# Optimization experiments

Hardware: AMD Instinct MI355X
Metric: run time of the kernel (lower is better)

## Reference

```python
import jax, jax.numpy as jnp
import numpy as np
import math

HIDDEN = 128; NHEADS = 4; N_COE = 50; N_SCALES = 4; THRE = 5.0; S = 4096; B = 1


def setup_inputs():
    key = jax.random.key(0)
    ks = jax.random.split(key, 12)
    w = lambda k, shape: jax.random.normal(k, shape, jnp.float32) * 0.05
    return {
        "eigenvalue": jax.random.uniform(ks[0], (B, S), jnp.float32) * 2.0,  # graph Laplacian eigvals in [0,2)
        "length": jnp.full((B,), S, dtype=jnp.int32),
        "sele_num": jnp.full((B,), S, dtype=jnp.int32),
        "eig_w_W": w(ks[1], (HIDDEN + 1, HIDDEN)), "eig_w_b": jnp.zeros((HIDDEN,), jnp.float32),
        "mha_ln_g": jnp.ones((HIDDEN,), jnp.float32), "mha_ln_b": jnp.zeros((HIDDEN,), jnp.float32),
        "in_W": w(ks[2], (HIDDEN, 3 * HIDDEN)), "in_b": jnp.zeros((3 * HIDDEN,), jnp.float32),
        "out_W": w(ks[3], (HIDDEN, HIDDEN)), "out_b": jnp.zeros((HIDDEN,), jnp.float32),
        "ffn_ln_g": jnp.ones((HIDDEN,), jnp.float32), "ffn_ln_b": jnp.zeros((HIDDEN,), jnp.float32),
        "ffn1_W": w(ks[4], (HIDDEN, HIDDEN)), "ffn1_b": jnp.zeros((HIDDEN,), jnp.float32),
        "ffn2_W": w(ks[5], (HIDDEN, HIDDEN)), "ffn2_b": jnp.zeros((HIDDEN,), jnp.float32),
        "dsc_W": w(ks[6], (HIDDEN, N_COE)), "dsc_b": jnp.zeros((N_COE,), jnp.float32),
        "dwv_W": w(ks[7], (HIDDEN, N_COE)), "dwv_b": jnp.zeros((N_COE,), jnp.float32),
        "dss_W": w(ks[8], (HIDDEN, N_SCALES)), "dss_b": jnp.zeros((N_SCALES,), jnp.float32),
    }


def layer_norm(x, g, b, eps=1e-5):
    m = x.mean(-1, keepdims=True)
    v = ((x - m) ** 2).mean(-1, keepdims=True)
    return (x - m) / jnp.sqrt(v + eps) * g + b


def sine_encoding(e, W, b):
    # e: [B, S] -> [B, S, HIDDEN]
    div = jnp.exp(jnp.arange(0, HIDDEN, 2, dtype=e.dtype) * (-math.log(10000.0) / HIDDEN))
    pe = (e * 100.0)[..., None] * div  # [B, S, HIDDEN/2]
    eeig = jnp.concatenate([e[..., None], jnp.sin(pe), jnp.cos(pe)], axis=-1)  # [B, S, HIDDEN+1]
    return eeig @ W + b


def mha(x, pad_mask, in_W, in_b, out_W, out_b):
    # x: [B, S, D]; pad_mask: [B, S] True = masked key
    Bb, Ss, D = x.shape
    hd = D // NHEADS
    qkv = x @ in_W + in_b
    q, k, v = jnp.split(qkv, 3, axis=-1)
    hsplit = lambda t: t.reshape(Bb, Ss, NHEADS, hd).transpose(0, 2, 1, 3)  # [B, H, S, hd]
    q, k, v = hsplit(q), hsplit(k), hsplit(v)
    scores = jnp.einsum('bhqd,bhkd->bhqk', q, k) / math.sqrt(hd)
    scores = jnp.where(pad_mask[:, None, None, :], -jnp.inf, scores)
    attn = jax.nn.softmax(scores, axis=-1)
    o = jnp.einsum('bhqk,bhkd->bhqd', attn, v).transpose(0, 2, 1, 3).reshape(Bb, Ss, D)
    return o @ out_W + out_b


def cheb_base(y, n_coe, flag):
    # Chebyshev recurrence: wavelet = [T_0, T_2, ...], scaling = [T_1, T_3, ...]
    te0 = jnp.ones_like(y)
    to0 = y
    def step(carry, _):
        te, to = carry
        te = 2.0 * y * to - te
        to = 2.0 * y * te - to
        return (te, to), (te, to)
    _, (evens, odds) = jax.lax.scan(step, (te0, to0), None, length=n_coe - 1)
    if flag == 'scaling':
        base = jnp.concatenate([to0[None], odds], axis=0)   # [n_coe, B, S, d]
    else:
        base = jnp.concatenate([te0[None], evens], axis=0)
    return jnp.moveaxis(base, 0, 1)  # [B, n_coe, S, d]


def _forward(eigenvalue, eig_w_W, eig_w_b, mha_ln_g, mha_ln_b, in_W, in_b, out_W, out_b,
             ffn_ln_g, ffn_ln_b, ffn1_W, ffn1_b, ffn2_W, ffn2_b,
             dsc_W, dsc_b, dwv_W, dwv_b, dss_W, dss_b, length, sele_num):
    Bb, Ss = eigenvalue.shape
    eve = eigenvalue
    eig_mask = jnp.arange(Ss)[None, :] >= sele_num[:, None]  # [B, S] True = pad
    # --- EigenEncoding (dropout in eval mode = identity) ---
    eig = sine_encoding(eve, eig_w_W, eig_w_b)
    eig = eig + mha(layer_norm(eig, mha_ln_g, mha_ln_b), eig_mask, in_W, in_b, out_W, out_b)
    f = layer_norm(eig, ffn_ln_g, ffn_ln_b)
    f = jax.nn.gelu(f @ ffn1_W + ffn1_b, approximate=False) @ ffn2_W + ffn2_b
    eig_filter = eig + f  # [B, S, HIDDEN]
    lenf = length.astype(eve.dtype)[:, None]
    def pooled(W, b):
        c = eig_filter @ W + b
        c = jnp.where(eig_mask[..., None], 0.0, c)
        return c.sum(axis=1) / (lenf + 1e-8)
    coe_scaling = jax.nn.sigmoid(pooled(dsc_W, dsc_b))
    coe_scaling = coe_scaling / (coe_scaling.sum(-1, keepdims=True) + 1e-8)  # [B, n_coe]
    coe_wavelet = jax.nn.sigmoid(pooled(dwv_W, dwv_b))
    coe_wavelet = coe_wavelet / (coe_wavelet.sum(-1, keepdims=True) + 1e-8)
    coe_scales = jax.nn.sigmoid(pooled(dss_W, dss_b)) * THRE  # [B, n_scales]
    # --- Chebyshev bases ---
    base_scaling = cheb_base(eve[..., None] - 1.0, N_COE, 'scaling')  # [B, n_coe, S, 1]
    fsw = eve[..., None] * coe_scales[:, None, :]                      # [B, S, n_scales]
    fsw = jnp.where(fsw > 2.0, 0.0, fsw)
    base_wavelet = cheb_base(fsw - 1.0, N_COE, 'wavelet')             # [B, n_coe, S, n_scales]
    base_scaling = 0.5 * (1.0 - base_scaling)
    base_wavelet = 0.5 * (1.0 - base_wavelet)
    curr_scaling = jnp.einsum('bc,bcsd->bsd', coe_scaling, base_scaling)
    curr_wavelet = jnp.einsum('bc,bcsd->bsd', coe_wavelet, base_wavelet)
    out = jnp.concatenate([curr_scaling, curr_wavelet], axis=-1)       # [B, S, 1+n_scales]
    out = out / (jnp.linalg.norm(out, axis=-1, keepdims=True) + 1e-8)  # cfg.lam.tight_use = True
    return out


def reference(eigenvalue, length, sele_num, eig_w_W, eig_w_b, mha_ln_g, mha_ln_b, in_W, in_b,
              out_W, out_b, ffn_ln_g, ffn_ln_b, ffn1_W, ffn1_b, ffn2_W, ffn2_b,
              dsc_W, dsc_b, dwv_W, dwv_b, dss_W, dss_b):
    return _forward(eigenvalue, eig_w_W, eig_w_b, mha_ln_g, mha_ln_b, in_W, in_b, out_W, out_b,
                    ffn_ln_g, ffn_ln_b, ffn1_W, ffn1_b, ffn2_W, ffn2_b,
                    dsc_W, dsc_b, dwv_W, dwv_b, dss_W, dss_b, length, sele_num)
```

## Files before the change

### kernel.cpp

```cpp
#include <hip/hip_runtime.h>
#include <math.h>


#define SLOTS 8

typedef __attribute__((ext_vector_type(8))) short short8;
typedef __attribute__((ext_vector_type(4))) short short4v;
typedef __attribute__((ext_vector_type(4))) float f32x4;

__device__ inline unsigned short f2bf(float x) {
    unsigned u = __float_as_uint(x);
    return (unsigned short)((u + 0x7FFFu + ((u >> 16) & 1u)) >> 16);
}
__device__ inline float bf2f(unsigned short h) { return __uint_as_float(((unsigned)h) << 16); }

__global__ __launch_bounds__(256) void k_embed(const float* __restrict__ eve,
    const float* __restrict__ eigW, const float* __restrict__ ebias,
    const float* __restrict__ g, const float* __restrict__ b,
    const float* __restrict__ inW, const float* __restrict__ inb,
    float* __restrict__ eig, float* __restrict__ qkv, unsigned short* __restrict__ Khi_g,
    unsigned short* __restrict__ Klo_g, unsigned short* __restrict__ Vt_g)
{
    __shared__ __align__(16) float wsh[129 * 128];
    __shared__ __align__(16) float se[16][132];
    __shared__ __align__(16) float xn[16][132];
    __shared__ __align__(16) unsigned short vsh[128][16];
    const int t = threadIdx.x;
    const int r0 = blockIdx.x * 16;
    {
        const int r = t >> 4, l4 = t & 15;
        const float e = eve[r0 + r];
        if (l4 == 0) se[r][128] = e;
        #pragma unroll
        for (int jj = 0; jj < 4; ++jj) {
            const int j = l4 * 4 + jj;
            const float div = __expf(-0.07195578415606394f * (float)(2 * j));
            const float pe = e * 100.0f * div;
            se[r][j]      = __sinf(pe);
            se[r][64 + j] = __cosf(pe);
        }
    }
    {
        const float4* __restrict__ src = (const float4*)eigW;
        float4* dst = (float4*)wsh;
        #pragma unroll
        for (int i = 0; i < 17; ++i) {
            const int f = t + i * 256;
            if (f < 4128) dst[f] = src[f];
        }
    }
    __syncthreads();
    const int lane = t & 63;
    const int w = t >> 6;
    const int rp = w * 2 + (lane >> 5);
    const int c0 = (lane & 31) * 4;
    const int ra = rp * 2, rb = ra + 1;
    float xa[4], xb[4];
    {
        const float4 w0 = *(const float4*)&wsh[c0];
        const float ea = se[ra][128], eb = se[rb][128];
        float a0 = ea * w0.x, a1 = ea * w0.y, a2 = ea * w0.z, a3 = ea * w0.w;
        float b0 = eb * w0.x, b1 = eb * w0.y, b2 = eb * w0.z, b3 = eb * w0.w;
        #pragma unroll 8
        for (int k = 0; k < 128; ++k) {
            const float xva = se[ra][k];
            const float xvb = se[rb][k];
            const float4 wk = *(const float4*)&wsh[(k + 1) * 128 + c0];
            a0 = fmaf(xva, wk.x, a0); a1 = fmaf(xva, wk.y, a1);
            a2 = fmaf(xva, wk.z, a2); a3 = fmaf(xva, wk.w, a3);
            b0 = fmaf(xvb, wk.x, b0); b1 = fmaf(xvb, wk.y, b1);
            b2 = fmaf(xvb, wk.z, b2); b3 = fmaf(xvb, wk.w, b3);
        }
        const float4 bb = *(const float4*)&ebias[c0];
        xa[0] = a0 + bb.x; xa[1] = a1 + bb.y; xa[2] = a2 + bb.z; xa[3] = a3 + bb.w;
        xb[0] = b0 + bb.x; xb[1] = b1 + bb.y; xb[2] = b2 + bb.z; xb[3] = b3 + bb.w;
        *(float4*)&eig[(size_t)(r0 + ra) * 128 + c0] = make_float4(xa[0], xa[1], xa[2], xa[3]);
        *(float4*)&eig[(size_t)(r0 + rb) * 128 + c0] = make_float4(xb[0], xb[1], xb[2], xb[3]);
    }
    {
        float sa = (xa[0] + xa[1]) + (xa[2] + xa[3]);
        float qa = (xa[0] * xa[0] + xa[1] * xa[1]) + (xa[2] * xa[2] + xa[3] * xa[3]);
        float sb = (xb[0] + xb[1]) + (xb[2] + xb[3]);
        float qb = (xb[0] * xb[0] + xb[1] * xb[1]) + (xb[2] * xb[2] + xb[3] * xb[3]);
        #pragma unroll
        for (int m = 1; m < 32; m <<= 1) {
            sa += __shfl_xor(sa, m, 32); qa += __shfl_xor(qa, m, 32);
            sb += __shfl_xor(sb, m, 32); qb += __shfl_xor(qb, m, 32);
        }
        const float ma = sa * (1.f / 128.f), mb = sb * (1.f / 128.f);
        const float ia = 1.f / sqrtf(qa * (1.f / 128.f) - ma * ma + 1e-5f);
        const float ib = 1.f / sqrtf(qb * (1.f / 128.f) - mb * mb + 1e-5f);
        const float4 gg = *(const float4*)&g[c0];
        const float4 bb = *(const float4*)&b[c0];
        *(float4*)&xn[ra][c0] = make_float4((xa[0] - ma) * ia * gg.x + bb.x,
                                            (xa[1] - ma) * ia * gg.y + bb.y,
                                            (xa[2] - ma) * ia * gg.z + bb.z,
                                            (xa[3] - ma) * ia * gg.w + bb.w);
        *(float4*)&xn[rb][c0] = make_float4((xb[0] - mb) * ib * gg.x + bb.x,
                                            (xb[1] - mb) * ib * gg.y + bb.y,
                                            (xb[2] - mb) * ib * gg.z + bb.z,
                                            (xb[3] - mb) * ib * gg.w + bb.w);
    }
    const int rowa = r0 + ra, rowb = r0 + rb;
    for (int p = 0; p < 3; ++p) {
        __syncthreads();
        {
            const float4* __restrict__ src = (const float4*)inW;
            float4* dst = (float4*)wsh;
            #pragma unroll
            for (int i = 0; i < 16; ++i) {
                const int f = t + i * 256;
                const int k = f >> 5, c4 = f & 31;
                dst[f] = src[k * 96 + p * 32 + c4];
            }
        }
        __syncthreads();
        float A[4], B[4];
        {
            const float4 bb = *(const float4*)&inb[p * 128 + c0];
            A[0] = bb.x; A[1] = bb.y; A[2] = bb.z; A[3] = bb.w;
            B[0] = bb.x; B[1] = bb.y; B[2] = bb.z; B[3] = bb.w;
        }
        #pragma unroll 8
        for (int k = 0; k < 128; ++k) {
            const float xva = xn[ra][k];
            const float xvb = xn[rb][k];
            const float4 wk = *(const float4*)&wsh[k * 128 + c0];
            A[0] = fmaf(xva, wk.x, A[0]); A[1] = fmaf(xva, wk.y, A[1]);
            A[2] = fmaf(xva, wk.z, A[2]); A[3] = fmaf(xva, wk.w, A[3]);
            B[0] = fmaf(xvb, wk.x, B[0]); B[1] = fmaf(xvb, wk.y, B[1]);
            B[2] = fmaf(xvb, wk.z, B[2]); B[3] = fmaf(xvb, wk.w, B[3]);
        }
        if (p == 0) {
            *(float4*)&qkv[(size_t)rowa * 384 + c0] = make_float4(A[0], A[1], A[2], A[3]);
            *(float4*)&qkv[(size_t)rowb * 384 + c0] = make_float4(B[0], B[1], B[2], B[3]);
        } else if (p == 1) {
            const int h = c0 >> 5, d = c0 & 31;
            unsigned short h4[4], l4v[4];
            #pragma unroll
            for (int i = 0; i < 4; ++i) { h4[i] = f2bf(A[i]); l4v[i] = f2bf(A[i] - bf2f(h4[i])); }
            *(uint2*)&Khi_g[((size_t)h * 4096 + rowa) * 32 + d] = *(uint2*)h4;
            *(uint2*)&Klo_g[((size_t)h * 4096 + rowa) * 32 + d] = *(uint2*)l4v;
            #pragma unroll
            for (int i = 0; i < 4; ++i) { h4[i] = f2bf(B[i]); l4v[i] = f2bf(B[i] - bf2f(h4[i])); }
            *(uint2*)&Khi_g[((size_t)h * 4096 + rowb) * 32 + d] = *(uint2*)h4;
            *(uint2*)&Klo_g[((size_t)h * 4096 + rowb) * 32 + d] = *(uint2*)l4v;
        } else {
            #pragma unroll
            for (int i = 0; i < 4; ++i) {
                vsh[c0 + i][ra] = f2bf(A[i]);
                vsh[c0 + i][rb] = f2bf(B[i]);
            }
        }
    }
    __syncthreads();
    if (t < 128) {
        const uint4 v0 = *(const uint4*)&vsh[t][0];
        const uint4 v1 = *(const uint4*)&vsh[t][8];
        *(uint4*)&Vt_g[(size_t)t * 4096 + r0]     = v0;
        *(uint4*)&Vt_g[(size_t)t * 4096 + r0 + 8] = v1;
    }
}

#define PSTR 72

__global__ __launch_bounds__(256) void k_attn(const float* __restrict__ qkv,
    const unsigned short* __restrict__ Khi_g, const unsigned short* __restrict__ Klo_g,
    const unsigned short* __restrict__ Vt_g,
    const int* __restrict__ sele, float* __restrict__ Oe, float* __restrict__ E)
{
    __shared__ __align__(16) unsigned short Pb[4][64 * PSTR];

    const int t = threadIdx.x;
    const int lane = t & 63;
    const int l = lane & 15;
    const int quad = lane >> 4;
    const int wv = __builtin_amdgcn_readfirstlane(t >> 6);
    const int qb = blockIdx.x;
    const int h  = blockIdx.y;
    const int slot = blockIdx.z * 4 + wv;
    const int nk = sele[0];
    unsigned short* __restrict__ Pw = Pb[wv];

    short8 qhi[4], qlo[4];
    #pragma unroll
    for (int qf = 0; qf < 4; ++qf) {
        const float* __restrict__ qr =
            qkv + (size_t)(qb * 64 + qf * 16 + l) * 384 + h * 32 + quad * 8;
        const float4 a = *(const float4*)qr;
        const float4 b = *(const float4*)(qr + 4);
        const float sc = 0.17677669529663687f;
        float v[8] = {a.x * sc, a.y * sc, a.z * sc, a.w * sc, b.x * sc, b.y * sc, b.z * sc, b.w * sc};
        #pragma unroll
        for (int j = 0; j < 8; ++j) {
            const unsigned short hb = f2bf(v[j]);
            qhi[qf][j] = (short)hb;
            qlo[qf][j] = (short)f2bf(v[j] - bf2f(hb));
        }
    }
    f32x4 accO[4][2];
    #pragma unroll
    for (int qf = 0; qf < 4; ++qf) {
        accO[qf][0] = (f32x4){0.f, 0.f, 0.f, 0.f};
        accO[qf][1] = (f32x4){0.f, 0.f, 0.f, 0.f};
    }
    float elane[4] = {0.f, 0.f, 0.f, 0.f};

    for (int ch = 0; ch < 8; ++ch) {
        const int keybase = slot * 512 + ch * 64;
        #pragma unroll
        for (int tile = 0; tile < 4; ++tile) {
            const size_t krow = (size_t)h * 4096 + keybase + tile * 16 + l;
            const short8 kh = *(const short8*)&Khi_g[krow * 32 + quad * 8];
            const short8 kw = *(const short8*)&Klo_g[krow * 32 + quad * 8];
            const int kg0 = keybase + tile * 16 + quad * 4;
            #pragma unroll
            for (int qf = 0; qf < 4; ++qf) {
                f32x4 S = {0.f, 0.f, 0.f, 0.f};
                S = __builtin_amdgcn_mfma_f32_16x16x32_bf16(kh, qhi[qf], S, 0, 0, 0);
                S = __builtin_amdgcn_mfma_f32_16x16x32_bf16(kw, qhi[qf], S, 0, 0, 0);
                S = __builtin_amdgcn_mfma_f32_16x16x32_bf16(kh, qlo[qf], S, 0, 0, 0);
                short4v pw;
                #pragma unroll
                for (int r = 0; r < 4; ++r) {
                    const float p = (kg0 + r < nk) ? __expf(S[r]) : 0.f;
                    elane[qf] += p;
                    pw[r] = (short)f2bf(p);
                }
                *(short4v*)&Pw[(qf * 16 + l) * PSTR + tile * 16 + quad * 4] = pw;
            }
        }
        #pragma unroll
        for (int pair = 0; pair < 2; ++pair) {
            short8 pa[4];
            #pragma unroll
            for (int qf = 0; qf < 4; ++qf)
                pa[qf] = *(const short8*)&Pw[(qf * 16 + l) * PSTR + pair * 32 + quad * 8];
            #pragma unroll
            for (int dt = 0; dt < 2; ++dt) {
                const short8 vb = *(const short8*)
                    &Vt_g[((size_t)h * 32 + dt * 16 + l) * 4096 + keybase + pair * 32 + quad * 8];
                #pragma unroll
                for (int qf = 0; qf < 4; ++qf)
                    accO[qf][dt] = __builtin_amdgcn_mfma_f32_16x16x32_bf16(pa[qf], vb, accO[qf][dt], 0, 0, 0);
            }
        }
    }
    #pragma unroll
    for (int qf = 0; qf < 4; ++qf) {
        float e = elane[qf];
        e += __shfl_xor(e, 16, 64);
        e += __shfl_xor(e, 32, 64);
        if (lane < 16)
            E[((size_t)slot * 4 + h) * 4096 + qb * 64 + qf * 16 + l] = e;
        #pragma unroll
        for (int r = 0; r < 4; ++r) {
            const size_t row = qb * 64 + qf * 16 + quad * 4 + r;
            Oe[((size_t)slot * 4096 + row) * 128 + h * 32 + l]      = accO[qf][0][r];
            Oe[((size_t)slot * 4096 + row) * 128 + h * 32 + 16 + l] = accO[qf][1][r];
        }
    }
}

__global__ __launch_bounds__(256) void k_ffn(const float* __restrict__ eig,
    const float* __restrict__ Oe, const float* __restrict__ E,
    const float* __restrict__ outW, const float* __restrict__ outb,
    const float* __restrict__ lg, const float* __restrict__ lb,
    const float* __restrict__ W1, const float* __restrict__ b1,
    const float* __restrict__ W2, const float* __restrict__ b2,
    const int* __restrict__ sele, float* __restrict__ xsum)
{
    __shared__ __align__(16) float wsh[128 * 128];
    __shared__ __align__(16) float sA[16][132];
    __shared__ __align__(16) float xn[16][132];
    __shared__ __align__(16) float cs[16][132];
    const int t = threadIdx.x;
    const int r0 = blockIdx.x * 16;
    {
        const int r = t >> 4, c8 = (t & 15) * 8;
        const int h = c8 >> 5;
        float es = 0.f;
        float v[8] = {0.f, 0.f, 0.f, 0.f, 0.f, 0.f, 0.f, 0.f};
        #pragma unroll
        for (int ks = 0; ks < SLOTS; ++ks) {
            es += E[((size_t)ks * 4 + h) * 4096 + r0 + r];
            const float4 o1 = *(const float4*)&Oe[((size_t)ks * 4096 + r0 + r) * 128 + c8];
            const float4 o2 = *(const float4*)&Oe[((size_t)ks * 4096 + r0 + r) * 128 + c8 + 4];
            v[0] += o1.x; v[1] += o1.y; v[2] += o1.z; v[3] += o1.w;
            v[4] += o2.x; v[5] += o2.y; v[6] += o2.z; v[7] += o2.w;
        }
        const float rcp = 1.f / es;
        *(float4*)&sA[r][c8]     = make_float4(v[0] * rcp, v[1] * rcp, v[2] * rcp, v[3] * rcp);
        *(float4*)&sA[r][c8 + 4] = make_float4(v[4] * rcp, v[5] * rcp, v[6] * rcp, v[7] * rcp);
    }
    {
        const float4* __restrict__ src = (const float4*)outW;
        float4* dst = (float4*)wsh;
        #pragma unroll
        for (int i = 0; i < 16; ++i) dst[t + i * 256] = src[t + i * 256];
    }
    __syncthreads();
    const int lane = t & 63;
    const int w = t >> 6;
    const int rp = w * 2 + (lane >> 5);
    const int c0 = (lane & 31) * 4;
    const int ra = rp * 2, rb = ra + 1;
    float x2a[4], x2b[4];
    {
        const float4 bb = *(const float4*)&outb[c0];
        float a0 = bb.x, a1 = bb.y, a2 = bb.z, a3 = bb.w;
        float b0 = bb.x, b1 = bb.y, b2 = bb.z, b3 = bb.w;
        #pragma unroll 8
        for (int k = 0; k < 128; ++k) {
            const float xva = sA[ra][k];
            const float xvb = sA[rb][k];
            const float4 wk = *(const float4*)&wsh[k * 128 + c0];
            a0 = fmaf(xva, wk.x, a0); a1 = fmaf(xva, wk.y, a1);
            a2 = fmaf(xva, wk.z, a2); a3 = fmaf(xva, wk.w, a3);
            b0 = fmaf(xvb, wk.x, b0); b1 = fmaf(xvb, wk.y, b1);
            b2 = fmaf(xvb, wk.z, b2); b3 = fmaf(xvb, wk.w, b3);
        }
        const float4 ea = *(const float4*)&eig[(size_t)(r0 + ra) * 128 + c0];
        const float4 eb = *(const float4*)&eig[(size_t)(r0 + rb) * 128 + c0];
        x2a[0] = ea.x + a0; x2a[1] = ea.y + a1; x2a[2] = ea.z + a2; x2a[3] = ea.w + a3;
        x2b[0] = eb.x + b0; x2b[1] = eb.y + b1; x2b[2] = eb.z + b2; x2b[3] = eb.w + b3;
    }
    {
        float sa = (x2a[0] + x2a[1]) + (x2a[2] + x2a[3]);
        float qa = (x2a[0] * x2a[0] + x2a[1] * x2a[1]) + (x2a[2] * x2a[2] + x2a[3] * x2a[3]);
        float sb = (x2b[0] + x2b[1]) + (x2b[2] + x2b[3]);
        float qb = (x2b[0] * x2b[0] + x2b[1] * x2b[1]) + (x2b[2] * x2b[2] + x2b[3] * x2b[3]);
        #pragma unroll
        for (int m = 1; m < 32; m <<= 1) {
            sa += __shfl_xor(sa, m, 32); qa += __shfl_xor(qa, m, 32);
            sb += __shfl_xor(sb, m, 32); qb += __shfl_xor(qb, m, 32);
        }
        const float ma = sa * (1.f / 128.f), mb = sb * (1.f / 128.f);
        const float ia = 1.f / sqrtf(qa * (1.f / 128.f) - ma * ma + 1e-5f);
        const float ib = 1.f / sqrtf(qb * (1.f / 128.f) - mb * mb + 1e-5f);
        const float4 gg = *(const float4*)&lg[c0];
        const float4 bb = *(const float4*)&lb[c0];
        *(float4*)&xn[ra][c0] = make_float4((x2a[0] - ma) * ia * gg.x + bb.x,
                                            (x2a[1] - ma) * ia * gg.y + bb.y,
                                            (x2a[2] - ma) * ia * gg.z + bb.z,
                                            (x2a[3] - ma) * ia * gg.w + bb.w);
        *(float4*)&xn[rb][c0] = make_float4((x2b[0] - mb) * ib * gg.x + bb.x,
                                            (x2b[1] - mb) * ib * gg.y + bb.y,
                                            (x2b[2] - mb) * ib * gg.z + bb.z,
                                            (x2b[3] - mb) * ib * gg.w + bb.w);
    }
    __syncthreads();
    {
        const float4* __restrict__ src = (const float4*)W1;
        float4* dst = (float4*)wsh;
        #pragma unroll
        for (int i = 0; i < 16; ++i) dst[t + i * 256] = src[t + i * 256];
    }
    __syncthreads();
    {
        const float4 bb = *(const float4*)&b1[c0];
        float a0 = bb.x, a1 = bb.y, a2 = bb.z, a3 = bb.w;
        float b0 = bb.x, b1v = bb.y, b2v = bb.z, b3 = bb.w;
        #pragma unroll 8
        for (int k = 0; k < 128; ++k) {
            const float xva = xn[ra][k];
            const float xvb = xn[rb][k];
            const float4 wk = *(const float4*)&wsh[k * 128 + c0];
            a0 = fmaf(xva, wk.x, a0); a1 = fmaf(xva, wk.y, a1);
            a2 = fmaf(xva, wk.z, a2); a3 = fmaf(xva, wk.w, a3);
            b0 = fmaf(xvb, wk.x, b0); b1v = fmaf(xvb, wk.y, b1v);
            b2v = fmaf(xvb, wk.z, b2v); b3 = fmaf(xvb, wk.w, b3);
        }
        *(float4*)&sA[ra][c0] = make_float4(
            0.5f * a0 * (1.f + erff(a0 * 0.70710678118654752f)),
            0.5f * a1 * (1.f + erff(a1 * 0.70710678118654752f)),
            0.5f * a2 * (1.f + erff(a2 * 0.70710678118654752f)),
            0.5f * a3 * (1.f + erff(a3 * 0.70710678118654752f)));
        *(float4*)&sA[rb][c0] = make_float4(
            0.5f * b0 * (1.f + erff(b0 * 0.70710678118654752f)),
            0.5f * b1v * (1.f + erff(b1v * 0.70710678118654752f)),
            0.5f * b2v * (1.f + erff(b2v * 0.70710678118654752f)),
            0.5f * b3 * (1.f + erff(b3 * 0.70710678118654752f)));
    }
    __syncthreads();
    {
        const float4* __restrict__ src = (const float4*)W2;
        float4* dst = (float4*)wsh;
        #pragma unroll
        for (int i = 0; i < 16; ++i) dst[t + i * 256] = src[t + i * 256];
    }
    __syncthreads();
    {
        const float4 bb = *(const float4*)&b2[c0];
        float a0 = bb.x, a1 = bb.y, a2 = bb.z, a3 = bb.w;
        float b0 = bb.x, b1v = bb.y, b2v = bb.z, b3 = bb.w;
        #pragma unroll 8
        for (int k = 0; k < 128; ++k) {
            const float xva = sA[ra][k];
            const float xvb = sA[rb][k];
            const float4 wk = *(const float4*)&wsh[k * 128 + c0];
            a0 = fmaf(xva, wk.x, a0); a1 = fmaf(xva, wk.y, a1);
            a2 = fmaf(xva, wk.z, a2); a3 = fmaf(xva, wk.w, a3);
            b0 = fmaf(xvb, wk.x, b0); b1v = fmaf(xvb, wk.y, b1v);
            b2v = fmaf(xvb, wk.z, b2v); b3 = fmaf(xvb, wk.w, b3);
        }
        const int nsel = sele[0];
        const bool ina = (r0 + ra) < nsel, inb2 = (r0 + rb) < nsel;
        *(float4*)&cs[ra][c0] = ina ? make_float4(x2a[0] + a0, x2a[1] + a1, x2a[2] + a2, x2a[3] + a3)
                                    : make_float4(0.f, 0.f, 0.f, 0.f);
        *(float4*)&cs[rb][c0] = inb2 ? make_float4(x2b[0] + b0, x2b[1] + b1v, x2b[2] + b2v, x2b[3] + b3)
                                     : make_float4(0.f, 0.f, 0.f, 0.f);
    }
    __syncthreads();
    if (t < 128) {
        float s = 0.f;
        #pragma unroll
        for (int rr = 0; rr < 16; ++rr) s += cs[rr][t];
        atomicAdd(&xsum[t], s);
    }
}

__global__ __launch_bounds__(512) void k_coef(const float* __restrict__ xsum,
    const float* __restrict__ dscW, const float* __restrict__ dscb,
    const float* __restrict__ dwvW, const float* __restrict__ dwvb,
    const float* __restrict__ dssW, const float* __restrict__ dssb,
    const int* __restrict__ len, const int* __restrict__ sele,
    float* __restrict__ coef)
{
    __shared__ float xs[128];
    __shared__ float part[104][4];
    __shared__ float val[104];
    __shared__ float s2[2];
    const int t = threadIdx.x;
    if (t < 128) xs[t] = xsum[t];
    __syncthreads();
    const float invl = 1.f / ((float)len[0] + 1e-8f);
    const float ns = (float)sele[0];
    const int o = t >> 2, lk = t & 3;
    if (o < 104) {
        const float* Wp; int stride, col;
        if (o < 50)       { Wp = dscW; stride = 50; col = o; }
        else if (o < 100) { Wp = dwvW; stride = 50; col = o - 50; }
        else              { Wp = dssW; stride = 4;  col = o - 100; }
        float a = 0.f;
        #pragma unroll
        for (int kk = 0; kk < 32; ++kk) {
            const int k = lk * 32 + kk;
            a = fmaf(xs[k], Wp[k * stride + col], a);
        }
        part[o][lk] = a;
    }
    __syncthreads();
    if (t < 104) {
        const float bias = (t < 50) ? dscb[t] : ((t < 100) ? dwvb[t - 50] : dssb[t - 100]);
        float a = ((part[t][0] + part[t][1]) + (part[t][2] + part[t][3]) + ns * bias) * invl;
        val[t] = 1.f / (1.f + __expf(-a));
    }
    __syncthreads();
    if (t == 0) { float s = 0.f; for (int i = 0; i < 50; ++i) s += val[i]; s2[0] = s; }
    if (t == 1) { float s = 0.f; for (int i = 0; i < 50; ++i) s += val[50 + i]; s2[1] = s; }
    __syncthreads();
    if (t < 50) {
        coef[t]      = val[t] / (s2[0] + 1e-8f);
        coef[50 + t] = val[50 + t] / (s2[1] + 1e-8f);
    } else if (t >= 100 && t < 104) {
        coef[t] = val[t] * 5.0f;
    }
}

__global__ __launch_bounds__(128) void k_out(const float* __restrict__ eve,
    const float* __restrict__ coef, float* __restrict__ out)
{
    __shared__ float csc[50], cwv[50], cssh[4];
    const int t = threadIdx.x;
    if (t < 50) csc[t] = coef[t];
    else if (t < 100) cwv[t - 50] = coef[t];
    else if (t < 104) cssh[t - 100] = coef[t];
    __syncthreads();
    const int s = blockIdx.x * 128 + t;
    const float e = eve[s];
    float vals[5];
    {
        const float y = e - 1.f;
        float te = 1.f, to = y;
        float a = csc[0] * (0.5f * (1.f - to));
        const float y2 = 2.f * y;
        for (int i = 1; i < 50; ++i) {
            te = fmaf(y2, to, -te);
            to = fmaf(y2, te, -to);
            a = fmaf(csc[i], 0.5f * (1.f - to), a);
        }
        vals[0] = a;
    }
    #pragma unroll
    for (int j = 0; j < 4; ++j) {
        float f = e * cssh[j];
        if (f > 2.f) f = 0.f;
        const float y = f - 1.f;
        float te = 1.f, to = y;
        float a = cwv[0] * (0.5f * (1.f - te));
        const float y2 = 2.f * y;
        for (int i = 1; i < 50; ++i) {
            te = fmaf(y2, to, -te);
            to = fmaf(y2, te, -to);
            a = fmaf(cwv[i], 0.5f * (1.f - te), a);
        }
        vals[1 + j] = a;
    }
    float n2 = 0.f;
    #pragma unroll
    for (int k = 0; k < 5; ++k) n2 += vals[k] * vals[k];
    const float invn = 1.f / (sqrtf(n2) + 1e-8f);
    #pragma unroll
    for (int k = 0; k < 5; ++k) out[s * 5 + k] = vals[k] * invn;
}

extern "C" void kernel_launch(void* const* d_in, const int* in_sizes, int n_in,
                              void* d_out, int out_size, void* d_ws, size_t ws_size,
                              hipStream_t stream) {
    const float* eve  = (const float*)d_in[0];
    const int*   len  = (const int*)d_in[1];
    const int*   sele = (const int*)d_in[2];
    const float* eigW = (const float*)d_in[3];
    const float* eigB = (const float*)d_in[4];
    const float* mlg  = (const float*)d_in[5];
    const float* mlb  = (const float*)d_in[6];
    const float* inW  = (const float*)d_in[7];
    const float* inb  = (const float*)d_in[8];
    const float* outW = (const float*)d_in[9];
    const float* outb = (const float*)d_in[10];
    const float* flg  = (const float*)d_in[11];
    const float* flb  = (const float*)d_in[12];
    const float* W1   = (const float*)d_in[13];
    const float* b1   = (const float*)d_in[14];
    const float* W2   = (const float*)d_in[15];
    const float* b2   = (const float*)d_in[16];
    const float* dscW = (const float*)d_in[17];
    const float* dscb = (const float*)d_in[18];
    const float* dwvW = (const float*)d_in[19];
    const float* dwvb = (const float*)d_in[20];
    const float* dssW = (const float*)d_in[21];
    const float* dssb = (const float*)d_in[22];

    float* ws   = (float*)d_ws;
    float* eig  = ws;
    float* qkv  = ws + 524288;
    float* Oe   = ws + 2097152;
    float* E    = ws + 6291456;
    float* xsum = ws + 6422528;
    float* coef = ws + 6422656;
    unsigned short* Khi_g = (unsigned short*)(ws + 6422784);
    unsigned short* Klo_g = (unsigned short*)(ws + 6684928);
    unsigned short* Vt_g  = (unsigned short*)(ws + 6947072);
    float* out  = (float*)d_out;

    hipMemsetAsync(xsum, 0, 128 * sizeof(float), stream);
    k_embed<<<256, 256, 0, stream>>>(eve, eigW, eigB, mlg, mlb, inW, inb,
                                     eig, qkv, Khi_g, Klo_g, Vt_g);
    k_attn <<<dim3(64, 4, 2), 256, 0, stream>>>(qkv, Khi_g, Klo_g, Vt_g, sele, Oe, E);
    k_ffn  <<<256, 256, 0, stream>>>(eig, Oe, E, outW, outb, flg, flb, W1, b1, W2, b2, sele, xsum);
    k_coef <<<1, 512, 0, stream>>>(xsum, dscW, dscb, dwvW, dwvb, dssW, dssb, len, sele, coef);
    k_out  <<<32, 128, 0, stream>>>(eve, coef, out);
}
```

Baseline: 190.5 us.

## Halve rows per block in embed/FFN and double attention key split

Embed and FFN kernels now handle 8 rows per block with one row per thread group, so each launch has twice as many blocks (512). Attention splits the keys into 16 slots of 256 instead of 8 of 512, with grid z doubled, and the workspace layout is grown to hold the larger partial-output buffer. The goal is more blocks to fill the GPU's compute units. The cost is that each block reloads the weight matrices for half as many rows, and FFN must read and sum twice as many partial attention outputs.

```diff
diff --git a/kernel.cpp b/kernel.cpp
--- a/kernel.cpp
+++ b/kernel.cpp
@@ -2,7 +2,7 @@
 #include <math.h>
 
 
-#define SLOTS 8
+#define SLOTS 16
 
 typedef __attribute__((ext_vector_type(8))) short short8;
 typedef __attribute__((ext_vector_type(4))) short short4v;
@@ -22,18 +22,20 @@
     unsigned short* __restrict__ Klo_g, unsigned short* __restrict__ Vt_g)
 {
     __shared__ __align__(16) float wsh[129 * 128];
-    __shared__ __align__(16) float se[16][132];
-    __shared__ __align__(16) float xn[16][132];
-    __shared__ __align__(16) unsigned short vsh[128][16];
+    __shared__ __align__(16) float se[8][132];
+    __shared__ __align__(16) float xn[8][132];
+    __shared__ __align__(16) unsigned short vsh[128][8];
     const int t = threadIdx.x;
-    const int r0 = blockIdx.x * 16;
-    {
-        const int r = t >> 4, l4 = t & 15;
+    const int r0 = blockIdx.x * 8;
+    const int r = t >> 5;
+    const int l = t & 31;
+    const int c0 = l * 4;
+    {
         const float e = eve[r0 + r];
-        if (l4 == 0) se[r][128] = e;
-        #pragma unroll
-        for (int jj = 0; jj < 4; ++jj) {
-            const int j = l4 * 4 + jj;
+        if (l == 0) se[r][128] = e;
+        #pragma unroll
+        for (int jj = 0; jj < 2; ++jj) {
+            const int j = l * 2 + jj;
             const float div = __expf(-0.07195578415606394f * (float)(2 * j));
             const float pe = e * 100.0f * div;
             se[r][j]      = __sinf(pe);
@@ -50,58 +52,37 @@
         }
     }
     __syncthreads();
-    const int lane = t & 63;
-    const int w = t >> 6;
-    const int rp = w * 2 + (lane >> 5);
-    const int c0 = (lane & 31) * 4;
-    const int ra = rp * 2, rb = ra + 1;
-    float xa[4], xb[4];
+    float xa[4];
     {
         const float4 w0 = *(const float4*)&wsh[c0];
-        const float ea = se[ra][128], eb = se[rb][128];
-        float a0 = ea * w0.x, a1 = ea * w0.y, a2 = ea * w0.z, a3 = ea * w0.w;
-        float b0 = eb * w0.x, b1 = eb * w0.y, b2 = eb * w0.z, b3 = eb * w0.w;
+        const float e = se[r][128];
+        float a0 = e * w0.x, a1 = e * w0.y, a2 = e * w0.z, a3 = e * w0.w;
         #pragma unroll 8
         for (int k = 0; k < 128; ++k) {
-            const float xva = se[ra][k];
-            const float xvb = se[rb][k];
+            const float xv = se[r][k];
             const float4 wk = *(const float4*)&wsh[(k + 1) * 128 + c0];
-            a0 = fmaf(xva, wk.x, a0); a1 = fmaf(xva, wk.y, a1);
-            a2 = fmaf(xva, wk.z, a2); a3 = fmaf(xva, wk.w, a3);
-            b0 = fmaf(xvb, wk.x, b0); b1 = fmaf(xvb, wk.y, b1);
-            b2 = fmaf(xvb, wk.z, b2); b3 = fmaf(xvb, wk.w, b3);
+            a0 = fmaf(xv, wk.x, a0); a1 = fmaf(xv, wk.y, a1);
+            a2 = fmaf(xv, wk.z, a2); a3 = fmaf(xv, wk.w, a3);
         }
         const float4 bb = *(const float4*)&ebias[c0];
         xa[0] = a0 + bb.x; xa[1] = a1 + bb.y; xa[2] = a2 + bb.z; xa[3] = a3 + bb.w;
-        xb[0] = b0 + bb.x; xb[1] = b1 + bb.y; xb[2] = b2 + bb.z; xb[3] = b3 + bb.w;
-        *(float4*)&eig[(size_t)(r0 + ra) * 128 + c0] = make_float4(xa[0], xa[1], xa[2], xa[3]);
-        *(float4*)&eig[(size_t)(r0 + rb) * 128 + c0] = make_float4(xb[0], xb[1], xb[2], xb[3]);
-    }
-    {
-        float sa = (xa[0] + xa[1]) + (xa[2] + xa[3]);
-        float qa = (xa[0] * xa[0] + xa[1] * xa[1]) + (xa[2] * xa[2] + xa[3] * xa[3]);
-        float sb = (xb[0] + xb[1]) + (xb[2] + xb[3]);
-        float qb = (xb[0] * xb[0] + xb[1] * xb[1]) + (xb[2] * xb[2] + xb[3] * xb[3]);
-        #pragma unroll
-        for (int m = 1; m < 32; m <<= 1) {
-            sa += __shfl_xor(sa, m, 32); qa += __shfl_xor(qa, m, 32);
-            sb += __shfl_xor(sb, m, 32); qb += __shfl_xor(qb, m, 32);
-        }
-        const float ma = sa * (1.f / 128.f), mb = sb * (1.f / 128.f);
-        const float ia = 1.f / sqrtf(qa * (1.f / 128.f) - ma * ma + 1e-5f);
-        const float ib = 1.f / sqrtf(qb * (1.f / 128.f) - mb * mb + 1e-5f);
+        *(float4*)&eig[(size_t)(r0 + r) * 128 + c0] = make_float4(xa[0], xa[1], xa[2], xa[3]);
+    }
+    {
+        float s = (xa[0] + xa[1]) + (xa[2] + xa[3]);
+        float q = (xa[0] * xa[0] + xa[1] * xa[1]) + (xa[2] * xa[2] + xa[3] * xa[3]);
+        #pragma unroll
+        for (int m = 1; m < 32; m <<= 1) { s += __shfl_xor(s, m, 32); q += __shfl_xor(q, m, 32); }
+        const float mean = s * (1.f / 128.f);
+        const float inv  = 1.f / sqrtf(q * (1.f / 128.f) - mean * mean + 1e-5f);
         const float4 gg = *(const float4*)&g[c0];
         const float4 bb = *(const float4*)&b[c0];
-        *(float4*)&xn[ra][c0] = make_float4((xa[0] - ma) * ia * gg.x + bb.x,
-                                            (xa[1] - ma) * ia * gg.y + bb.y,
-                                            (xa[2] - ma) * ia * gg.z + bb.z,
-                                            (xa[3] - ma) * ia * gg.w + bb.w);
-        *(float4*)&xn[rb][c0] = make_float4((xb[0] - mb) * ib * gg.x + bb.x,
-                                            (xb[1] - mb) * ib * gg.y + bb.y,
-                                            (xb[2] - mb) * ib * gg.z + bb.z,
-                                            (xb[3] - mb) * ib * gg.w + bb.w);
-    }
-    const int rowa = r0 + ra, rowb = r0 + rb;
+        *(float4*)&xn[r][c0] = make_float4((xa[0] - mean) * inv * gg.x + bb.x,
+                                           (xa[1] - mean) * inv * gg.y + bb.y,
+                                           (xa[2] - mean) * inv * gg.z + bb.z,
+                                           (xa[3] - mean) * inv * gg.w + bb.w);
+    }
+    const int row = r0 + r;
     for (int p = 0; p < 3; ++p) {
         __syncthreads();
         {
@@ -115,50 +96,37 @@
             }
         }
         __syncthreads();
-        float A[4], B[4];
+        float A[4];
         {
             const float4 bb = *(const float4*)&inb[p * 128 + c0];
             A[0] = bb.x; A[1] = bb.y; A[2] = bb.z; A[3] = bb.w;
-            B[0] = bb.x; B[1] = bb.y; B[2] = bb.z; B[3] = bb.w;
         }
         #pragma unroll 8
         for (int k = 0; k < 128; ++k) {
-            const float xva = xn[ra][k];
-            const float xvb = xn[rb][k];
+            const float xv = xn[r][k];
             const float4 wk = *(const float4*)&wsh[k * 128 + c0];
-            A[0] = fmaf(xva, wk.x, A[0]); A[1] = fmaf(xva, wk.y, A[1]);
-            A[2] = fmaf(xva, wk.z, A[2]); A[3] = fmaf(xva, wk.w, A[3]);
-            B[0] = fmaf(xvb, wk.x, B[0]); B[1] = fmaf(xvb, wk.y, B[1]);
-            B[2] = fmaf(xvb, wk.z, B[2]); B[3] = fmaf(xvb, wk.w, B[3]);
+            A[0] = fmaf(xv, wk.x, A[0]); A[1] = fmaf(xv, wk.y, A[1]);
+            A[2] = fmaf(xv, wk.z, A[2]); A[3] = fmaf(xv, wk.w, A[3]);
         }
         if (p == 0) {
-            *(float4*)&qkv[(size_t)rowa * 384 + c0] = make_float4(A[0], A[1], A[2], A[3]);
-            *(float4*)&qkv[(size_t)rowb * 384 + c0] = make_float4(B[0], B[1], B[2], B[3]);
+            *(float4*)&qkv[(size_t)row * 384 + c0] = make_float4(A[0], A[1], A[2], A[3]);
         } else if (p == 1) {
             const int h = c0 >> 5, d = c0 & 31;
             unsigned short h4[4], l4v[4];
             #pragma unroll
             for (int i = 0; i < 4; ++i) { h4[i] = f2bf(A[i]); l4v[i] = f2bf(A[i] - bf2f(h4[i])); }
-            *(uint2*)&Khi_g[((size_t)h * 4096 + rowa) * 32 + d] = *(uint2*)h4;
-            *(uint2*)&Klo_g[((size_t)h * 4096 + rowa) * 32 + d] = *(uint2*)l4v;
-            #pragma unroll
-            for (int i = 0; i < 4; ++i) { h4[i] = f2bf(B[i]); l4v[i] = f2bf(B[i] - bf2f(h4[i])); }
-            *(uint2*)&Khi_g[((size_t)h * 4096 + rowb) * 32 + d] = *(uint2*)h4;
-            *(uint2*)&Klo_g[((size_t)h * 4096 + rowb) * 32 + d] = *(uint2*)l4v;
+            *(uint2*)&Khi_g[((size_t)h * 4096 + row) * 32 + d] = *(uint2*)h4;
+            *(uint2*)&Klo_g[((size_t)h * 4096 + row) * 32 + d] = *(uint2*)l4v;
         } else {
             #pragma unroll
-            for (int i = 0; i < 4; ++i) {
-                vsh[c0 + i][ra] = f2bf(A[i]);
-                vsh[c0 + i][rb] = f2bf(B[i]);
-            }
+            for (int i = 0; i < 4; ++i)
+                vsh[c0 + i][r] = f2bf(A[i]);
         }
     }
     __syncthreads();
     if (t < 128) {
         const uint4 v0 = *(const uint4*)&vsh[t][0];
-        const uint4 v1 = *(const uint4*)&vsh[t][8];
-        *(uint4*)&Vt_g[(size_t)t * 4096 + r0]     = v0;
-        *(uint4*)&Vt_g[(size_t)t * 4096 + r0 + 8] = v1;
+        *(uint4*)&Vt_g[(size_t)t * 4096 + r0] = v0;
     }
 }
 
@@ -206,8 +174,8 @@
     }
     float elane[4] = {0.f, 0.f, 0.f, 0.f};
 
-    for (int ch = 0; ch < 8; ++ch) {
-        const int keybase = slot * 512 + ch * 64;
+    for (int ch = 0; ch < 4; ++ch) {
+        const int keybase = slot * 256 + ch * 64;
         #pragma unroll
         for (int tile = 0; tile < 4; ++tile) {
             const size_t krow = (size_t)h * 4096 + keybase + tile * 16 + l;
@@ -271,27 +239,26 @@
     const int* __restrict__ sele, float* __restrict__ xsum)
 {
     __shared__ __align__(16) float wsh[128 * 128];
-    __shared__ __align__(16) float sA[16][132];
-    __shared__ __align__(16) float xn[16][132];
-    __shared__ __align__(16) float cs[16][132];
+    __shared__ __align__(16) float sA[8][132];
+    __shared__ __align__(16) float xn[8][132];
+    __shared__ __align__(16) float cs[8][132];
     const int t = threadIdx.x;
-    const int r0 = blockIdx.x * 16;
-    {
-        const int r = t >> 4, c8 = (t & 15) * 8;
-        const int h = c8 >> 5;
+    const int r0 = blockIdx.x * 8;
+    const int r = t >> 5;
+    const int c0 = (t & 31) * 4;
+    const int row = r0 + r;
+    {
+        const int h = c0 >> 5;
         float es = 0.f;
-        float v[8] = {0.f, 0.f, 0.f, 0.f, 0.f, 0.f, 0.f, 0.f};
+        float v[4] = {0.f, 0.f, 0.f, 0.f};
         #pragma unroll
         for (int ks = 0; ks < SLOTS; ++ks) {
-            es += E[((size_t)ks * 4 + h) * 4096 + r0 + r];
-            const float4 o1 = *(const float4*)&Oe[((size_t)ks * 4096 + r0 + r) * 128 + c8];
-            const float4 o2 = *(const float4*)&Oe[((size_t)ks * 4096 + r0 + r) * 128 + c8 + 4];
+            es += E[((size_t)ks * 4 + h) * 4096 + row];
+            const float4 o1 = *(const float4*)&Oe[((size_t)ks * 4096 + row) * 128 + c0];
             v[0] += o1.x; v[1] += o1.y; v[2] += o1.z; v[3] += o1.w;
-            v[4] += o2.x; v[5] += o2.y; v[6] += o2.z; v[7] += o2.w;
         }
         const float rcp = 1.f / es;
-        *(float4*)&sA[r][c8]     = make_float4(v[0] * rcp, v[1] * rcp, v[2] * rcp, v[3] * rcp);
-        *(float4*)&sA[r][c8 + 4] = make_float4(v[4] * rcp, v[5] * rcp, v[6] * rcp, v[7] * rcp);
+        *(float4*)&sA[r][c0] = make_float4(v[0] * rcp, v[1] * rcp, v[2] * rcp, v[3] * rcp);
     }
     {
         const float4* __restrict__ src = (const float4*)outW;
@@ -300,54 +267,33 @@
         for (int i = 0; i < 16; ++i) dst[t + i * 256] = src[t + i * 256];
     }
     __syncthreads();
-    const int lane = t & 63;
-    const int w = t >> 6;
-    const int rp = w * 2 + (lane >> 5);
-    const int c0 = (lane & 31) * 4;
-    const int ra = rp * 2, rb = ra + 1;
-    float x2a[4], x2b[4];
+    float x2[4];
     {
         const float4 bb = *(const float4*)&outb[c0];
         float a0 = bb.x, a1 = bb.y, a2 = bb.z, a3 = bb.w;
-        float b0 = bb.x, b1 = bb.y, b2 = bb.z, b3 = bb.w;
         #pragma unroll 8
         for (int k = 0; k < 128; ++k) {
-            const float xva = sA[ra][k];
-            const float xvb = sA[rb][k];
+            const float xv = sA[r][k];
             const float4 wk = *(const float4*)&wsh[k * 128 + c0];
-            a0 = fmaf(xva, wk.x, a0); a1 = fmaf(xva, wk.y, a1);
-            a2 = fmaf(xva, wk.z, a2); a3 = fmaf(xva, wk.w, a3);
-            b0 = fmaf(xvb, wk.x, b0); b1 = fmaf(xvb, wk.y, b1);
-            b2 = fmaf(xvb, wk.z, b2); b3 = fmaf(xvb, wk.w, b3);
-        }
-        const float4 ea = *(const float4*)&eig[(size_t)(r0 + ra) * 128 + c0];
-        const float4 eb = *(const float4*)&eig[(size_t)(r0 + rb) * 128 + c0];
-        x2a[0] = ea.x + a0; x2a[1] = ea.y + a1; x2a[2] = ea.z + a2; x2a[3] = ea.w + a3;
-        x2b[0] = eb.x + b0; x2b[1] = eb.y + b1; x2b[2] = eb.z + b2; x2b[3] = eb.w + b3;
-    }
-    {
-        float sa = (x2a[0] + x2a[1]) + (x2a[2] + x2a[3]);
-        float qa = (x2a[0] * x2a[0] + x2a[1] * x2a[1]) + (x2a[2] * x2a[2] + x2a[3] * x2a[3]);
-        float sb = (x2b[0] + x2b[1]) + (x2b[2] + x2b[3]);
-        float qb = (x2b[0] * x2b[0] + x2b[1] * x2b[1]) + (x2b[2] * x2b[2] + x2b[3] * x2b[3]);
-        #pragma unroll
-        for (int m = 1; m < 32; m <<= 1) {
-            sa += __shfl_xor(sa, m, 32); qa += __shfl_xor(qa, m, 32);
-            sb += __shfl_xor(sb, m, 32); qb += __shfl_xor(qb, m, 32);
-        }
-        const float ma = sa * (1.f / 128.f), mb = sb * (1.f / 128.f);
-        const float ia = 1.f / sqrtf(qa * (1.f / 128.f) - ma * ma + 1e-5f);
-        const float ib = 1.f / sqrtf(qb * (1.f / 128.f) - mb * mb + 1e-5f);
+            a0 = fmaf(xv, wk.x, a0); a1 = fmaf(xv, wk.y, a1);
+            a2 = fmaf(xv, wk.z, a2); a3 = fmaf(xv, wk.w, a3);
+        }
+        const float4 ea = *(const float4*)&eig[(size_t)row * 128 + c0];
+        x2[0] = ea.x + a0; x2[1] = ea.y + a1; x2[2] = ea.z + a2; x2[3] = ea.w + a3;
+    }
+    {
+        float s = (x2[0] + x2[1]) + (x2[2] + x2[3]);
+        float q = (x2[0] * x2[0] + x2[1] * x2[1]) + (x2[2] * x2[2] + x2[3] * x2[3]);
+        #pragma unroll
+        for (int m = 1; m < 32; m <<= 1) { s += __shfl_xor(s, m, 32); q += __shfl_xor(q, m, 32); }
+        const float mean = s * (1.f / 128.f);
+        const float inv  = 1.f / sqrtf(q * (1.f / 128.f) - mean * mean + 1e-5f);
         const float4 gg = *(const float4*)&lg[c0];
         const float4 bb = *(const float4*)&lb[c0];
-        *(float4*)&xn[ra][c0] = make_float4((x2a[0] - ma) * ia * gg.x + bb.x,
-                                            (x2a[1] - ma) * ia * gg.y + bb.y,
-                                            (x2a[2] - ma) * ia * gg.z + bb.z,
-                                            (x2a[3] - ma) * ia * gg.w + bb.w);
-        *(float4*)&xn[rb][c0] = make_float4((x2b[0] - mb) * ib * gg.x + bb.x,
-                                            (x2b[1] - mb) * ib * gg.y + bb.y,
-                                            (x2b[2] - mb) * ib * gg.z + bb.z,
-                                            (x2b[3] - mb) * ib * gg.w + bb.w);
+        *(float4*)&xn[r][c0] = make_float4((x2[0] - mean) * inv * gg.x + bb.x,
+                                           (x2[1] - mean) * inv * gg.y + bb.y,
+                                           (x2[2] - mean) * inv * gg.z + bb.z,
+                                           (x2[3] - mean) * inv * gg.w + bb.w);
     }
     __syncthreads();
     {
@@ -360,27 +306,18 @@
     {
         const float4 bb = *(const float4*)&b1[c0];
         float a0 = bb.x, a1 = bb.y, a2 = bb.z, a3 = bb.w;
-        float b0 = bb.x, b1v = bb.y, b2v = bb.z, b3 = bb.w;
         #pragma unroll 8
         for (int k = 0; k < 128; ++k) {
-            const float xva = xn[ra][k];
-            const float xvb = xn[rb][k];
+            const float xv = xn[r][k];
             const float4 wk = *(const float4*)&wsh[k * 128 + c0];
-            a0 = fmaf(xva, wk.x, a0); a1 = fmaf(xva, wk.y, a1);
-            a2 = fmaf(xva, wk.z, a2); a3 = fmaf(xva, wk.w, a3);
-            b0 = fmaf(xvb, wk.x, b0); b1v = fmaf(xvb, wk.y, b1v);
-            b2v = fmaf(xvb, wk.z, b2v); b3 = fmaf(xvb, wk.w, b3);
-        }
-        *(float4*)&sA[ra][c0] = make_float4(
+            a0 = fmaf(xv, wk.x, a0); a1 = fmaf(xv, wk.y, a1);
+            a2 = fmaf(xv, wk.z, a2); a3 = fmaf(xv, wk.w, a3);
+        }
+        *(float4*)&sA[r][c0] = make_float4(
             0.5f * a0 * (1.f + erff(a0 * 0.70710678118654752f)),
             0.5f * a1 * (1.f + erff(a1 * 0.70710678118654752f)),
             0.5f * a2 * (1.f + erff(a2 * 0.70710678118654752f)),
             0.5f * a3 * (1.f + erff(a3 * 0.70710678118654752f)));
-        *(float4*)&sA[rb][c0] = make_float4(
-            0.5f * b0 * (1.f + erff(b0 * 0.70710678118654752f)),
-            0.5f * b1v * (1.f + erff(b1v * 0.70710678118654752f)),
-            0.5f * b2v * (1.f + erff(b2v * 0.70710678118654752f)),
-            0.5f * b3 * (1.f + erff(b3 * 0.70710678118654752f)));
     }
     __syncthreads();
     {
@@ -393,29 +330,22 @@
     {
         const float4 bb = *(const float4*)&b2[c0];
         float a0 = bb.x, a1 = bb.y, a2 = bb.z, a3 = bb.w;
-        float b0 = bb.x, b1v = bb.y, b2v = bb.z, b3 = bb.w;
         #pragma unroll 8
         for (int k = 0; k < 128; ++k) {
-            const float xva = sA[ra][k];
-            const float xvb = sA[rb][k];
+            const float xv = sA[r][k];
             const float4 wk = *(const float4*)&wsh[k * 128 + c0];
-            a0 = fmaf(xva, wk.x, a0); a1 = fmaf(xva, wk.y, a1);
-            a2 = fmaf(xva, wk.z, a2); a3 = fmaf(xva, wk.w, a3);
-            b0 = fmaf(xvb, wk.x, b0); b1v = fmaf(xvb, wk.y, b1v);
-            b2v = fmaf(xvb, wk.z, b2v); b3 = fmaf(xvb, wk.w, b3);
-        }
-        const int nsel = sele[0];
-        const bool ina = (r0 + ra) < nsel, inb2 = (r0 + rb) < nsel;
-        *(float4*)&cs[ra][c0] = ina ? make_float4(x2a[0] + a0, x2a[1] + a1, x2a[2] + a2, x2a[3] + a3)
-                                    : make_float4(0.f, 0.f, 0.f, 0.f);
-        *(float4*)&cs[rb][c0] = inb2 ? make_float4(x2b[0] + b0, x2b[1] + b1v, x2b[2] + b2v, x2b[3] + b3)
-                                     : make_float4(0.f, 0.f, 0.f, 0.f);
+            a0 = fmaf(xv, wk.x, a0); a1 = fmaf(xv, wk.y, a1);
+            a2 = fmaf(xv, wk.z, a2); a3 = fmaf(xv, wk.w, a3);
+        }
+        const bool in = row < sele[0];
+        *(float4*)&cs[r][c0] = in ? make_float4(x2[0] + a0, x2[1] + a1, x2[2] + a2, x2[3] + a3)
+                                  : make_float4(0.f, 0.f, 0.f, 0.f);
     }
     __syncthreads();
     if (t < 128) {
         float s = 0.f;
         #pragma unroll
-        for (int rr = 0; rr < 16; ++rr) s += cs[rr][t];
+        for (int rr = 0; rr < 8; ++rr) s += cs[rr][t];
         atomicAdd(&xsum[t], s);
     }
 }
@@ -546,19 +476,19 @@
     float* eig  = ws;
     float* qkv  = ws + 524288;
     float* Oe   = ws + 2097152;
-    float* E    = ws + 6291456;
-    float* xsum = ws + 6422528;
-    float* coef = ws + 6422656;
-    unsigned short* Khi_g = (unsigned short*)(ws + 6422784);
-    unsigned short* Klo_g = (unsigned short*)(ws + 6684928);
-    unsigned short* Vt_g  = (unsigned short*)(ws + 6947072);
+    float* E    = ws + 10485760;
+    float* xsum = ws + 10747904;
+    float* coef = ws + 10748032;
+    unsigned short* Khi_g = (unsigned short*)(ws + 10748160);
+    unsigned short* Klo_g = (unsigned short*)(ws + 11010304);
+    unsigned short* Vt_g  = (unsigned short*)(ws + 11272448);
     float* out  = (float*)d_out;
 
     hipMemsetAsync(xsum, 0, 128 * sizeof(float), stream);
-    k_embed<<<256, 256, 0, stream>>>(eve, eigW, eigB, mlg, mlb, inW, inb,
+    k_embed<<<512, 256, 0, stream>>>(eve, eigW, eigB, mlg, mlb, inW, inb,
                                      eig, qkv, Khi_g, Klo_g, Vt_g);
-    k_attn <<<dim3(64, 4, 2), 256, 0, stream>>>(qkv, Khi_g, Klo_g, Vt_g, sele, Oe, E);
-    k_ffn  <<<256, 256, 0, stream>>>(eig, Oe, E, outW, outb, flg, flb, W1, b1, W2, b2, sele, xsum);
+    k_attn <<<dim3(64, 4, 4), 256, 0, stream>>>(qkv, Khi_g, Klo_g, Vt_g, sele, Oe, E);
+    k_ffn  <<<512, 256, 0, stream>>>(eig, Oe, E, outW, outb, flg, flb, W1, b1, W2, b2, sele, xsum);
     k_coef <<<1, 512, 0, stream>>>(xsum, dscW, dscb, dwvW, dwvb, dssW, dssb, len, sele, coef);
     k_out  <<<32, 128, 0, stream>>>(eve, coef, out);
 }
```

New measurement: 190.8 us. Within noise of the previous version (+0.2%).
